# Kernel optimization log

Measured on AMD Instinct MI355X. Metric: run time of the kernel, lower is better.

Reference implementation:

```python
import math
import jax, jax.numpy as jnp
import numpy as np

B, S, D, H = 4, 1024, 1024, 16
DK = D // H
NEG = jnp.float32(-1e32)
EPS = 1e-5


def setup_inputs() -> dict:
    key = jax.random.key(0)
    ks = jax.random.split(key, 10)
    s = 1.0 / math.sqrt(D)
    return {
        "query": jax.random.normal(ks[0], (B, S, D), jnp.float32),
        "key": jax.random.normal(ks[1], (B, S, D), jnp.float32),
        "values": jax.random.normal(ks[2], (B, S, D), jnp.float32),
        "lens": jax.random.randint(ks[3], (B,), 0, S).astype(jnp.int32),
        "state_weight": jax.random.normal(ks[4], (1, H, S, S), jnp.float32),
        # params (kq_same=True -> k shares q_linear weights)
        "Wq": jax.random.normal(ks[5], (D, D), jnp.float32) * s,
        "bq": jnp.zeros((D,), jnp.float32),
        "Wv": jax.random.normal(ks[6], (D, D), jnp.float32) * s,
        "bv": jnp.zeros((D,), jnp.float32),
        "Wo": jax.random.normal(ks[7], (D, D), jnp.float32) * s,
        "bo": jnp.zeros((D,), jnp.float32),
        "gamma": jnp.ones((D,), jnp.float32),
        "beta": jnp.zeros((D,), jnp.float32),
    }


def reference(query, key, values, lens, state_weight, Wq, bq, Wv, bv, Wo, bo, gamma, beta):
    # eval-mode forward of DTransformerLayer (peek_cur=False -> strictly causal)
    b, s, d = query.shape
    mask = jnp.tril(jnp.ones((s, s), bool), -1)[None, None]  # [1,1,S,S]

    q = (query @ Wq + bq).reshape(b, s, H, DK).transpose(0, 2, 1, 3)   # bhsd
    k = (key @ Wq + bq).reshape(b, s, H, DK).transpose(0, 2, 1, 3)     # shared weights (kq_same)
    v = (values @ Wv + bv).reshape(b, s, H, DK).transpose(0, 2, 1, 3)

    scores = jnp.einsum('bhqd,bhkd->bhqk', q, k) / math.sqrt(DK)
    scores = jnp.where(mask, scores, NEG)
    scores = jnp.where(mask, scores + state_weight, NEG)
    attn = jax.nn.softmax(scores, axis=-1)
    attn = jnp.where(mask, attn, 0.0)  # fully-masked rows (row 0) -> zeros, matching torch

    ctx = jnp.einsum('bhqk,bhkd->bhqd', attn, v).transpose(0, 2, 1, 3).reshape(b, s, d)
    out = ctx @ Wo + bo

    x = query + out  # dropout is identity in eval
    mu = jnp.mean(x, axis=-1, keepdims=True)
    var = jnp.mean(jnp.square(x - mu), axis=-1, keepdims=True)
    return (x - mu) * jax.lax.rsqrt(var + EPS) * gamma + beta
```

## Files before the change

### kernel.cpp

```cpp
#include <hip/hip_runtime.h>

#define B_ 4
#define S_ 1024
#define D_ 1024
#define H_ 16
#define DK_ 64

typedef __attribute__((ext_vector_type(8))) short short8;
typedef __attribute__((ext_vector_type(4))) float f32x4;
typedef __attribute__((ext_vector_type(16))) float f32x16;

#define CBASE_PACK 0x100C090604020100ULL

static __device__ __forceinline__ unsigned bf16rne(float x) {
    unsigned b = __float_as_uint(x);
    return (b + 0x7FFFu + ((b >> 16) & 1u)) >> 16;
}

__global__ __launch_bounds__(256) void transpose_cvt3(
    const float* __restrict__ W0, const float* __restrict__ W1,
    const float* __restrict__ W2, ushort* __restrict__ T0,
    ushort* __restrict__ T1, ushort* __restrict__ T2)
{
    __shared__ float ts[32][33];
    const float* W = (blockIdx.z == 0) ? W0 : (blockIdx.z == 1) ? W1 : W2;
    ushort*     Wt = (blockIdx.z == 0) ? T0 : (blockIdx.z == 1) ? T1 : T2;
    const int t  = threadIdx.x;
    const int k0 = blockIdx.y * 32, n0 = blockIdx.x * 32;
    const int r  = t >> 3, c4 = (t & 7) * 4;
    const float4 v = *reinterpret_cast<const float4*>(&W[(size_t)(k0 + r) * 1024 + n0 + c4]);
    ts[r][c4] = v.x; ts[r][c4 + 1] = v.y; ts[r][c4 + 2] = v.z; ts[r][c4 + 3] = v.w;
    __syncthreads();
    ushort4 o;
    o.x = (ushort)bf16rne(ts[c4    ][r]);
    o.y = (ushort)bf16rne(ts[c4 + 1][r]);
    o.z = (ushort)bf16rne(ts[c4 + 2][r]);
    o.w = (ushort)bf16rne(ts[c4 + 3][r]);
    *reinterpret_cast<ushort4*>(&Wt[(size_t)(n0 + r) * 1024 + k0 + c4]) = o;
}

template<int MODE>
__global__ __launch_bounds__(256) void gemm_f32a(
    const float* __restrict__ Xf0, const float* __restrict__ Xf1,
    const ushort* __restrict__ Wt, const float* __restrict__ bias,
    void* __restrict__ out0, void* __restrict__ out1)
{
    __shared__ ushort As[2][64 * 64];
    __shared__ ushort Bs[2][128 * 64];

    const int t    = threadIdx.x;
    const int lane = t & 63;
    const int w    = t >> 6;

    const int cpx     = gridDim.x >> 3;
    const int logical = (blockIdx.x & 7) * cpx + (blockIdx.x >> 3);
    const int bm = logical >> 3;
    const int bn = logical & 7;

    const int srow   = lane >> 3;
    const int schunk = (lane & 7) ^ srow;

    const float* Xf = (MODE == 1 && bm >= 64) ? Xf1 : Xf0;
    const int rbase = (bm * 64) & 4095;
    const float* ap[2];
#pragma unroll
    for (int j = 0; j < 2; ++j)
        ap[j] = Xf + (size_t)(rbase + (j * 4 + w) * 8 + srow) * 1024 + schunk * 8;

    const ushort* bg[4];
#pragma unroll
    for (int j = 0; j < 4; ++j)
        bg[j] = Wt + (size_t)(bn * 128 + (j * 4 + w) * 8 + srow) * 1024 + schunk * 8;

    float4 aRx0, aRy0, aRx1, aRy1;

#define A_ISSUE(k0)                                                              \
    do {                                                                         \
        aRx0 = *reinterpret_cast<const float4*>(ap[0] + (k0));                   \
        aRy0 = *reinterpret_cast<const float4*>(ap[0] + (k0) + 4);               \
        aRx1 = *reinterpret_cast<const float4*>(ap[1] + (k0));                   \
        aRy1 = *reinterpret_cast<const float4*>(ap[1] + (k0) + 4);               \
    } while (0)

#define B_STAGE(buf, k0)                                                         \
    do {                                                                         \
        _Pragma("unroll")                                                        \
        for (int j = 0; j < 4; ++j)                                              \
            __builtin_amdgcn_global_load_lds(                                    \
                (__attribute__((address_space(1))) const void*)(bg[j] + (k0)),   \
                (__attribute__((address_space(3))) void*)&Bs[buf][(j * 4 + w) * 512], \
                16, 0, 0);                                                       \
    } while (0)

#define A_WRITE(buf)                                                             \
    do {                                                                         \
        union { unsigned u[4]; int4 v; } p0, p1;                                 \
        asm("v_cvt_pk_bf16_f32 %0, %1, %2" : "=v"(p0.u[0]) : "v"(aRx0.x), "v"(aRx0.y)); \
        asm("v_cvt_pk_bf16_f32 %0, %1, %2" : "=v"(p0.u[1]) : "v"(aRx0.z), "v"(aRx0.w)); \
        asm("v_cvt_pk_bf16_f32 %0, %1, %2" : "=v"(p0.u[2]) : "v"(aRy0.x), "v"(aRy0.y)); \
        asm("v_cvt_pk_bf16_f32 %0, %1, %2" : "=v"(p0.u[3]) : "v"(aRy0.z), "v"(aRy0.w)); \
        asm("v_cvt_pk_bf16_f32 %0, %1, %2" : "=v"(p1.u[0]) : "v"(aRx1.x), "v"(aRx1.y)); \
        asm("v_cvt_pk_bf16_f32 %0, %1, %2" : "=v"(p1.u[1]) : "v"(aRx1.z), "v"(aRx1.w)); \
        asm("v_cvt_pk_bf16_f32 %0, %1, %2" : "=v"(p1.u[2]) : "v"(aRy1.x), "v"(aRy1.y)); \
        asm("v_cvt_pk_bf16_f32 %0, %1, %2" : "=v"(p1.u[3]) : "v"(aRy1.z), "v"(aRy1.w)); \
        *reinterpret_cast<int4*>(&As[buf][((0 * 4 + w) * 64 + lane) * 8]) = p0.v; \
        *reinterpret_cast<int4*>(&As[buf][((1 * 4 + w) * 64 + lane) * 8]) = p1.v; \
    } while (0)

    const int fr = lane & 15;
    const int fk = lane >> 4;
    const int wm = w >> 1, wn = w & 1;

    f32x4 acc[2][4];
#pragma unroll
    for (int m = 0; m < 2; ++m)
#pragma unroll
        for (int n = 0; n < 4; ++n) acc[m][n] = (f32x4){0.f, 0.f, 0.f, 0.f};

    A_ISSUE(0);
    B_STAGE(0, 0);
    asm volatile("s_waitcnt vmcnt(4)" ::: "memory");
    A_WRITE(0);
    asm volatile("s_waitcnt lgkmcnt(0)" ::: "memory");

#pragma unroll 1
    for (int kt = 0; kt < 16; ++kt) {
        const int cur = kt & 1;
        if (kt + 1 < 16) {
            A_ISSUE((kt + 1) * 64);
            B_STAGE(cur ^ 1, (kt + 1) * 64);
            asm volatile("s_waitcnt vmcnt(8)" ::: "memory");
        } else {
            asm volatile("s_waitcnt vmcnt(0)" ::: "memory");
        }
        __builtin_amdgcn_s_barrier();
        __builtin_amdgcn_sched_barrier(0);
#pragma unroll
        for (int ks = 0; ks < 2; ++ks) {
            short8 af[2], bf[4];
#pragma unroll
            for (int m = 0; m < 2; ++m) {
                const int row = wm * 32 + m * 16 + fr;
                af[m] = *reinterpret_cast<const short8*>(
                    &As[cur][row * 64 + (((ks * 4 + fk) ^ (row & 7)) * 8)]);
            }
#pragma unroll
            for (int n = 0; n < 4; ++n) {
                const int row = wn * 64 + n * 16 + fr;
                bf[n] = *reinterpret_cast<const short8*>(
                    &Bs[cur][row * 64 + (((ks * 4 + fk) ^ (row & 7)) * 8)]);
            }
            __builtin_amdgcn_s_setprio(1);
#pragma unroll
            for (int m = 0; m < 2; ++m)
#pragma unroll
                for (int n = 0; n < 4; ++n)
                    acc[m][n] = __builtin_amdgcn_mfma_f32_16x16x32_bf16(
                        af[m], bf[n], acc[m][n], 0, 0, 0);
            __builtin_amdgcn_s_setprio(0);
        }
        if (kt + 1 < 16) {
            asm volatile("s_waitcnt vmcnt(4)" ::: "memory");
            A_WRITE(cur ^ 1);
            asm volatile("s_waitcnt lgkmcnt(0)" ::: "memory");
        }
        __builtin_amdgcn_sched_barrier(0);
        __builtin_amdgcn_s_barrier();
        __builtin_amdgcn_sched_barrier(0);
    }
#undef A_ISSUE
#undef B_STAGE
#undef A_WRITE

#pragma unroll
    for (int m = 0; m < 2; ++m) {
        const int row0 = bm * 64 + wm * 32 + m * 16 + fk * 4;
#pragma unroll
        for (int n = 0; n < 4; ++n) {
            const int col = bn * 128 + wn * 64 + n * 16 + fr;
            const float bc = bias[col];
            if (MODE == 1) {
                ushort* o = (row0 < 4096) ? (ushort*)out0 : (ushort*)out1;
                const float qs = (row0 < 4096) ? 0.125f : 1.0f;
                const int r0 = row0 & 4095;
                const int b_ = r0 >> 10, s0 = r0 & 1023;
                const int h  = col >> 6,  dk = col & 63;
#pragma unroll
                for (int j = 0; j < 4; ++j)
                    o[(((size_t)b_ * H_ + h) * S_ + s0 + j) * DK_ + dk] =
                        (ushort)bf16rne((acc[m][n][j] + bc) * qs);
            } else {
                ushort* o = (ushort*)out0;
                const int b_ = row0 >> 10, s0 = row0 & 1023;
                const int h  = col >> 6,   dk = col & 63;
                ushort4 pk;
                pk.x = (ushort)bf16rne(acc[m][n][0] + bc);
                pk.y = (ushort)bf16rne(acc[m][n][1] + bc);
                pk.z = (ushort)bf16rne(acc[m][n][2] + bc);
                pk.w = (ushort)bf16rne(acc[m][n][3] + bc);
                *reinterpret_cast<ushort4*>(
                    &o[(((size_t)b_ * H_ + h) * DK_ + dk) * S_ + s0]) = pk;
            }
        }
    }
}

__global__ __launch_bounds__(256) void gemm_bf16a(
    const ushort* __restrict__ X, const ushort* __restrict__ Wt,
    const float* __restrict__ bias, const float* __restrict__ resid,
    float* __restrict__ out)
{
    __shared__ ushort As[2][64 * 64];
    __shared__ ushort Bs[2][128 * 64];

    const int t    = threadIdx.x;
    const int lane = t & 63;
    const int w    = t >> 6;

    const int cpx     = gridDim.x >> 3;
    const int logical = (blockIdx.x & 7) * cpx + (blockIdx.x >> 3);
    const int bm = logical >> 3;
    const int bn = logical & 7;

    const int srow   = lane >> 3;
    const int schunk = (lane & 7) ^ srow;
    const ushort* ag[2];
    const ushort* bg[4];
#pragma unroll
    for (int j = 0; j < 2; ++j)
        ag[j] = X  + (size_t)(bm * 64 + (j * 4 + w) * 8 + srow) * 1024 + schunk * 8;
#pragma unroll
    for (int j = 0; j < 4; ++j)
        bg[j] = Wt + (size_t)(bn * 128 + (j * 4 + w) * 8 + srow) * 1024 + schunk * 8;

#define STAGE(buf, k0)                                                           \
    do {                                                                         \
        _Pragma("unroll")                                                        \
        for (int j = 0; j < 2; ++j)                                              \
            __builtin_amdgcn_global_load_lds(                                    \
                (__attribute__((address_space(1))) const void*)(ag[j] + (k0)),   \
                (__attribute__((address_space(3))) void*)&As[buf][(j * 4 + w) * 512], \
                16, 0, 0);                                                       \
        _Pragma("unroll")                                                        \
        for (int j = 0; j < 4; ++j)                                              \
            __builtin_amdgcn_global_load_lds(                                    \
                (__attribute__((address_space(1))) const void*)(bg[j] + (k0)),   \
                (__attribute__((address_space(3))) void*)&Bs[buf][(j * 4 + w) * 512], \
                16, 0, 0);                                                       \
    } while (0)

    const int fr = lane & 15;
    const int fk = lane >> 4;
    const int wm = w >> 1, wn = w & 1;

    f32x4 acc[2][4];
#pragma unroll
    for (int m = 0; m < 2; ++m)
#pragma unroll
        for (int n = 0; n < 4; ++n) acc[m][n] = (f32x4){0.f, 0.f, 0.f, 0.f};

    STAGE(0, 0);
#pragma unroll 1
    for (int kt = 0; kt < 16; ++kt) {
        const int cur = kt & 1;
        if (kt + 1 < 16) {
            STAGE(cur ^ 1, (kt + 1) * 64);
            asm volatile("s_waitcnt vmcnt(6)" ::: "memory");
        } else {
            asm volatile("s_waitcnt vmcnt(0)" ::: "memory");
        }
        __builtin_amdgcn_s_barrier();
        __builtin_amdgcn_sched_barrier(0);
#pragma unroll
        for (int ks = 0; ks < 2; ++ks) {
            short8 af[2], bf[4];
#pragma unroll
            for (int m = 0; m < 2; ++m) {
                const int row = wm * 32 + m * 16 + fr;
                af[m] = *reinterpret_cast<const short8*>(
                    &As[cur][row * 64 + (((ks * 4 + fk) ^ (row & 7)) * 8)]);
            }
#pragma unroll
            for (int n = 0; n < 4; ++n) {
                const int row = wn * 64 + n * 16 + fr;
                bf[n] = *reinterpret_cast<const short8*>(
                    &Bs[cur][row * 64 + (((ks * 4 + fk) ^ (row & 7)) * 8)]);
            }
            __builtin_amdgcn_s_setprio(1);
#pragma unroll
            for (int m = 0; m < 2; ++m)
#pragma unroll
                for (int n = 0; n < 4; ++n)
                    acc[m][n] = __builtin_amdgcn_mfma_f32_16x16x32_bf16(
                        af[m], bf[n], acc[m][n], 0, 0, 0);
            __builtin_amdgcn_s_setprio(0);
        }
        __builtin_amdgcn_sched_barrier(0);
        __builtin_amdgcn_s_barrier();
        __builtin_amdgcn_sched_barrier(0);
    }
#undef STAGE

#pragma unroll
    for (int m = 0; m < 2; ++m) {
        const int row0 = bm * 64 + wm * 32 + m * 16 + fk * 4;
#pragma unroll
        for (int n = 0; n < 4; ++n) {
            const int col = bn * 128 + wn * 64 + n * 16 + fr;
            const float bc = bias[col];
#pragma unroll
            for (int j = 0; j < 4; ++j) {
                const int row = row0 + j;
                out[(size_t)row * 1024 + col] =
                    acc[m][n][j] + bc + resid[(size_t)row * 1024 + col];
            }
        }
    }
}

__global__ __launch_bounds__(256) void attn_mfma(
    const ushort* __restrict__ Qh, const ushort* __restrict__ Kh,
    const ushort* __restrict__ Vt, const float* __restrict__ SW,
    ushort* __restrict__ ctxP, float2* __restrict__ ml)
{
    __shared__ ushort Ks[2][4096];
    __shared__ ushort Vs[2][4096];

    const int t    = threadIdx.x;
    const int lane = t & 63;
    const int w    = t >> 6;
    const int lg = (blockIdx.x & 7) * 160 + (blockIdx.x >> 3);
    const int b  = lg & 3;
    const int hc = lg >> 2;
    const int h  = hc / 20;
    const int ci = hc % 20;
    const int bh = b * 16 + h;
    int qb = 0;
#pragma unroll
    for (int q = 1; q < 8; ++q)
        if ((int)((CBASE_PACK >> (q * 8)) & 0xff) <= ci) qb = q;
    const int lc = ci - (int)((CBASE_PACK >> (qb * 8)) & 0xff);
    const int t0 = lc * 4;
    const int nt = min(4, 2 * qb + 2 - t0);

    const int ql = lane & 31;
    const int hi = lane >> 5;
    const int qrow = qb * 128 + ql * 4 + w;

    const ushort* Kg  = Kh + (size_t)bh * S_ * DK_;
    const ushort* Vg  = Vt + (size_t)bh * DK_ * S_;
    const float*  swp = SW + ((size_t)h * S_ + qrow) * S_;

    const ushort* kgp[2];
    const ushort* vgp[2];
#pragma unroll
    for (int j = 0; j < 2; ++j) {
        const int bb = w * 2 + j;
        const int g = bb >> 2, c = bb & 3;
        kgp[j] = Kg + (size_t)(g * 32 + ql) * DK_ + c * 16 + hi * 8;
        vgp[j] = Vg + (size_t)(g * 32 + ql) * S_  + c * 16 + hi * 8;
    }

#define ASTAGE(buf, k0)                                                          \
    do {                                                                         \
        _Pragma("unroll")                                                        \
        for (int j = 0; j < 2; ++j) {                                            \
            const int bb = w * 2 + j;                                            \
            __builtin_amdgcn_global_load_lds(                                    \
                (__attribute__((address_space(1))) const void*)(kgp[j] + (size_t)(k0) * DK_), \
                (__attribute__((address_space(3))) void*)&Ks[buf][bb * 512],     \
                16, 0, 0);                                                       \
            __builtin_amdgcn_global_load_lds(                                    \
                (__attribute__((address_space(1))) const void*)(vgp[j] + (k0)),  \
                (__attribute__((address_space(3))) void*)&Vs[buf][bb * 512],     \
                16, 0, 0);                                                       \
        }                                                                        \
    } while (0)

    short8 qf[4];
    {
        const ushort* Qg = Qh + ((size_t)bh * S_ + qrow) * DK_;
#pragma unroll
        for (int c = 0; c < 4; ++c) {
            union { int4 i; short8 s; } u;
            u.i = *reinterpret_cast<const int4*>(&Qg[c * 16 + hi * 8]);
            qf[c] = u.s;
        }
    }

    f32x16 accA, accB;
#pragma unroll
    for (int r = 0; r < 16; ++r) { accA[r] = 0.f; accB[r] = 0.f; }
    float mrow = -1e30f, lrow = 0.f;

    ASTAGE(0, t0 * 64);

#pragma unroll 1
    for (int kt = 0; kt < nt; ++kt) {
        const int cur = kt & 1;
        const int k0  = (t0 + kt) * 64;
        if (kt + 1 < nt) {
            ASTAGE(cur ^ 1, (t0 + kt + 1) * 64);
            asm volatile("s_waitcnt vmcnt(4)" ::: "memory");
        } else {
            asm volatile("s_waitcnt vmcnt(0)" ::: "memory");
        }
        __builtin_amdgcn_s_barrier();
        __builtin_amdgcn_sched_barrier(0);

        float swv[2][16];
#pragma unroll
        for (int g = 0; g < 2; ++g)
#pragma unroll
            for (int j = 0; j < 4; ++j) {
                const float4 v = *reinterpret_cast<const float4*>(
                    &swp[k0 + g * 32 + hi * 4 + j * 8]);
                swv[g][j * 4 + 0] = v.x; swv[g][j * 4 + 1] = v.y;
                swv[g][j * 4 + 2] = v.z; swv[g][j * 4 + 3] = v.w;
            }

        f32x16 sc[2];
        __builtin_amdgcn_s_setprio(1);
#pragma unroll
        for (int g = 0; g < 2; ++g) {
#pragma unroll
            for (int r = 0; r < 16; ++r) sc[g][r] = 0.f;
#pragma unroll
            for (int c = 0; c < 4; ++c) {
                const short8 kf = *reinterpret_cast<const short8*>(
                    &Ks[cur][((g * 4 + c) * 64 + lane) * 8]);
                sc[g] = __builtin_amdgcn_mfma_f32_32x32x16_bf16(kf, qf[c], sc[g], 0, 0, 0);
            }
        }
        __builtin_amdgcn_s_setprio(0);

        float pr[2][16];
        float tmax = -1e30f;
        if (t0 + kt >= 2 * qb) {
#pragma unroll
            for (int g = 0; g < 2; ++g)
#pragma unroll
                for (int r = 0; r < 16; ++r) {
                    const int key = k0 + g * 32 + (r & 3) + ((r >> 2) << 3) + (hi << 2);
                    const float s = (key < qrow) ? sc[g][r] + swv[g][r] : -1e30f;
                    pr[g][r] = s;
                    tmax = fmaxf(tmax, s);
                }
        } else {
#pragma unroll
            for (int g = 0; g < 2; ++g)
#pragma unroll
                for (int r = 0; r < 16; ++r) {
                    const float s = sc[g][r] + swv[g][r];
                    pr[g][r] = s;
                    tmax = fmaxf(tmax, s);
                }
        }
        tmax = fmaxf(tmax, __shfl_xor(tmax, 32, 64));
        const float mnew = fmaxf(mrow, tmax);
        const float corr = __expf(mrow - mnew);
        float psum = 0.f;
#pragma unroll
        for (int g = 0; g < 2; ++g)
#pragma unroll
            for (int r = 0; r < 16; ++r) {
                const float e = (pr[g][r] > -1e29f) ? __expf(pr[g][r] - mnew) : 0.f;
                pr[g][r] = e;
                psum += e;
            }
        psum += __shfl_xor(psum, 32, 64);
        lrow = lrow * corr + psum;
        mrow = mnew;
#pragma unroll
        for (int r = 0; r < 16; ++r) { accA[r] *= corr; accB[r] *= corr; }

        short8 paf[4];
#pragma unroll
        for (int g = 0; g < 2; ++g) {
            unsigned pk[8];
#pragma unroll
            for (int j = 0; j < 8; ++j) {
                unsigned r_;
                asm("v_cvt_pk_bf16_f32 %0, %1, %2"
                    : "=v"(r_) : "v"(pr[g][2 * j]), "v"(pr[g][2 * j + 1]));
                pk[j] = r_;
            }
            unsigned x0 = (unsigned)__shfl_xor((int)pk[0], 32, 64);
            unsigned x1 = (unsigned)__shfl_xor((int)pk[1], 32, 64);
            unsigned x2 = (unsigned)__shfl_xor((int)pk[2], 32, 64);
            unsigned x3 = (unsigned)__shfl_xor((int)pk[3], 32, 64);
            unsigned x4 = (unsigned)__shfl_xor((int)pk[4], 32, 64);
            unsigned x5 = (unsigned)__shfl_xor((int)pk[5], 32, 64);
            unsigned x6 = (unsigned)__shfl_xor((int)pk[6], 32, 64);
            unsigned x7 = (unsigned)__shfl_xor((int)pk[7], 32, 64);
            union { unsigned u[4]; short8 s; } a0, a1;
            a0.u[0] = hi ? x2 : pk[0];
            a0.u[1] = hi ? x3 : pk[1];
            a0.u[2] = hi ? pk[2] : x0;
            a0.u[3] = hi ? pk[3] : x1;
            a1.u[0] = hi ? x6 : pk[4];
            a1.u[1] = hi ? x7 : pk[5];
            a1.u[2] = hi ? pk[6] : x4;
            a1.u[3] = hi ? pk[7] : x5;
            paf[g * 2 + 0] = a0.s;
            paf[g * 2 + 1] = a1.s;
        }

        __builtin_amdgcn_s_setprio(1);
#pragma unroll
        for (int cc = 0; cc < 4; ++cc) {
            const short8 va = *reinterpret_cast<const short8*>(
                &Vs[cur][((0 * 4 + cc) * 64 + lane) * 8]);
            const short8 vb = *reinterpret_cast<const short8*>(
                &Vs[cur][((1 * 4 + cc) * 64 + lane) * 8]);
            accA = __builtin_amdgcn_mfma_f32_32x32x16_bf16(va, paf[cc], accA, 0, 0, 0);
            accB = __builtin_amdgcn_mfma_f32_32x32x16_bf16(vb, paf[cc], accB, 0, 0, 0);
        }
        __builtin_amdgcn_s_setprio(0);

        __builtin_amdgcn_sched_barrier(0);
        __builtin_amdgcn_s_barrier();
        __builtin_amdgcn_sched_barrier(0);
    }
#undef ASTAGE

    const float inv = (lrow > 0.f) ? 1.f / lrow : 0.f;
    ushort* crow_ = ctxP + ((size_t)(bh * 20 + ci) * 128 + (ql * 4 + w)) * 64;
#pragma unroll
    for (int g = 0; g < 4; ++g) {
        ushort4 oA, oB;
        oA.x = (ushort)bf16rne(accA[4 * g + 0] * inv);
        oA.y = (ushort)bf16rne(accA[4 * g + 1] * inv);
        oA.z = (ushort)bf16rne(accA[4 * g + 2] * inv);
        oA.w = (ushort)bf16rne(accA[4 * g + 3] * inv);
        oB.x = (ushort)bf16rne(accB[4 * g + 0] * inv);
        oB.y = (ushort)bf16rne(accB[4 * g + 1] * inv);
        oB.z = (ushort)bf16rne(accB[4 * g + 2] * inv);
        oB.w = (ushort)bf16rne(accB[4 * g + 3] * inv);
        *reinterpret_cast<ushort4*>(&crow_[g * 8 + hi * 4])      = oA;
        *reinterpret_cast<ushort4*>(&crow_[g * 8 + hi * 4 + 32]) = oB;
    }
    if (hi == 0) {
        float2 v; v.x = mrow; v.y = lrow;
        ml[(size_t)(bh * 20 + ci) * 128 + ql * 4 + w] = v;
    }
}

__global__ __launch_bounds__(256) void attn_merge(
    const ushort* __restrict__ ctxP, const float2* __restrict__ ml,
    ushort* __restrict__ ctx)
{
    const size_t idx = ((size_t)blockIdx.x * 256 + threadIdx.x) * 8;
    const int col = (int)(idx & 1023);
    const int row = (int)(idx >> 10);
    const int b = row >> 10, s = row & 1023;
    const int h = col >> 6, dk0 = col & 63;
    const int bh = b * 16 + h;
    const int qb = s >> 7, rl = s & 127;
    const int nch = (qb + 2) >> 1;
    const int cb  = (int)((CBASE_PACK >> (qb * 8)) & 0xff);

    float mm[4], ll[4];
    float m = -1e30f;
#pragma unroll
    for (int c = 0; c < 4; ++c)
        if (c < nch) {
            const float2 v = ml[(size_t)(bh * 20 + cb + c) * 128 + rl];
            mm[c] = v.x; ll[c] = v.y;
            m = fmaxf(m, v.x);
        }
    float wc[4], wsum = 0.f;
#pragma unroll
    for (int c = 0; c < 4; ++c)
        if (c < nch) { wc[c] = ll[c] * __expf(mm[c] - m); wsum += wc[c]; }
    const float inv = (wsum > 0.f) ? 1.f / wsum : 0.f;

    float o[8] = {0.f, 0.f, 0.f, 0.f, 0.f, 0.f, 0.f, 0.f};
#pragma unroll
    for (int c = 0; c < 4; ++c)
        if (c < nch) {
            union { int4 v; ushort u[8]; } p;
            p.v = *reinterpret_cast<const int4*>(
                &ctxP[((size_t)(bh * 20 + cb + c) * 128 + rl) * 64 + dk0]);
            const float wgt = wc[c] * inv;
#pragma unroll
            for (int i = 0; i < 8; ++i)
                o[i] += wgt * __uint_as_float((unsigned)p.u[i] << 16);
        }
    union { int4 v; ushort u[8]; } r;
#pragma unroll
    for (int i = 0; i < 8; ++i) r.u[i] = (ushort)bf16rne(o[i]);
    *reinterpret_cast<int4*>(ctx + idx) = r.v;
}

__global__ __launch_bounds__(256) void layernorm_k(
    const float* __restrict__ x, const float* __restrict__ gamma,
    const float* __restrict__ beta, float* __restrict__ out)
{
    const int row = blockIdx.x;
    const int t   = threadIdx.x;
    const float4 v = *reinterpret_cast<const float4*>(&x[(size_t)row * D_ + (t << 2)]);
    float sum = v.x + v.y + v.z + v.w;
    float sq  = v.x * v.x + v.y * v.y + v.z * v.z + v.w * v.w;
#pragma unroll
    for (int w = 1; w < 64; w <<= 1) {
        sum += __shfl_xor(sum, w, 64);
        sq  += __shfl_xor(sq,  w, 64);
    }
    __shared__ float red[8];
    const int wid = t >> 6;
    if ((t & 63) == 0) { red[wid] = sum; red[wid + 4] = sq; }
    __syncthreads();
    sum = red[0] + red[1] + red[2] + red[3];
    sq  = red[4] + red[5] + red[6] + red[7];
    const float mu  = sum * (1.f / 1024.f);
    const float var = sq * (1.f / 1024.f) - mu * mu;
    const float rs  = rsqrtf(var + 1e-5f);
    const float4 gm = *reinterpret_cast<const float4*>(&gamma[t << 2]);
    const float4 bt = *reinterpret_cast<const float4*>(&beta[t << 2]);
    float4 o;
    o.x = (v.x - mu) * rs * gm.x + bt.x;
    o.y = (v.y - mu) * rs * gm.y + bt.y;
    o.z = (v.z - mu) * rs * gm.z + bt.z;
    o.w = (v.w - mu) * rs * gm.w + bt.w;
    *reinterpret_cast<float4*>(&out[(size_t)row * D_ + (t << 2)]) = o;
}

extern "C" void kernel_launch(void* const* d_in, const int* in_sizes, int n_in,
                              void* d_out, int out_size, void* d_ws, size_t ws_size,
                              hipStream_t stream)
{
    const float* query  = (const float*)d_in[0];
    const float* key    = (const float*)d_in[1];
    const float* values = (const float*)d_in[2];
    const float* SW     = (const float*)d_in[4];
    const float* Wq     = (const float*)d_in[5];
    const float* bq     = (const float*)d_in[6];
    const float* Wv     = (const float*)d_in[7];
    const float* bv     = (const float*)d_in[8];
    const float* Wo     = (const float*)d_in[9];
    const float* bo     = (const float*)d_in[10];
    const float* gamma  = (const float*)d_in[11];
    const float* beta   = (const float*)d_in[12];

    char* ws = (char*)d_ws;
    const size_t MB = 1024 * 1024;
    ushort* Qh   = (ushort*)(ws);
    ushort* Kh   = (ushort*)(ws +  8 * MB);
    ushort* Vt   = (ushort*)(ws + 16 * MB);
    ushort* Wqt  = (ushort*)(ws + 24 * MB);
    ushort* Wvt  = (ushort*)(ws + 26 * MB);
    ushort* Wot  = (ushort*)(ws + 28 * MB);
    ushort* ctxP = (ushort*)(ws + 30 * MB);
    float2* ml   = (float2*)(ws + 52 * MB);
    ushort* ctxm = Qh;
    float*  xbf  = (float*)(ws + 8 * MB);

    const dim3 blk(256);

    transpose_cvt3<<<dim3(32, 32, 3), blk, 0, stream>>>(Wq, Wv, Wo, Wqt, Wvt, Wot);

    gemm_f32a<1><<<dim3(1024), blk, 0, stream>>>(query, key, Wqt, bq, Qh, Kh);
    gemm_f32a<2><<<dim3(512),  blk, 0, stream>>>(values, nullptr, Wvt, bv, Vt, nullptr);

    attn_mfma<<<dim3(1280), blk, 0, stream>>>(Qh, Kh, Vt, SW, ctxP, ml);
    attn_merge<<<dim3(2048), blk, 0, stream>>>(ctxP, ml, ctxm);

    gemm_bf16a<<<dim3(512), blk, 0, stream>>>(ctxm, Wot, bo, query, xbf);

    layernorm_k<<<dim3(4096), blk, 0, stream>>>(xbf, gamma, beta, (float*)d_out);
}
```

Before: 145.0 us.

## Fuse Q/K/V projections into one launch and rebalance causal attention chunking

The separate Q/K and V projection GEMM launches become a single kernel of 1536 blocks that picks its input, weight, bias and output layout from the block's row index. This removes one launch and lets the V tiles fill the machine alongside Q/K. The attention split-K decomposition changes from 20 chunks per head to 16, using packed lookup tables for query block, start tile and tile count. This reduces the block count and merge work and is meant to balance causal work per block better. The risk lies in the per-chunk tile counts and in the merge tables having to match the new partition exactly.

After: 127.7 us. 11.9% less time.

```diff
diff --git a/kernel.cpp b/kernel.cpp
--- a/kernel.cpp
+++ b/kernel.cpp
@@ -10,7 +10,11 @@
 typedef __attribute__((ext_vector_type(4))) float f32x4;
 typedef __attribute__((ext_vector_type(16))) float f32x16;
 
-#define CBASE_PACK 0x100C090604020100ULL
+#define QBPACK 0x7777666554433210ULL
+#define T0PACK 0xC840A50605040000ULL
+#define NTPACK 0x4444455665544642ULL
+#define CBPACK  0x0C09070503020100ULL
+#define NCHPACK 0x43222111U
 
 static __device__ __forceinline__ unsigned bf16rne(float x) {
     unsigned b = __float_as_uint(x);
@@ -39,11 +43,12 @@
     *reinterpret_cast<ushort4*>(&Wt[(size_t)(n0 + r) * 1024 + k0 + c4]) = o;
 }
 
-template<int MODE>
-__global__ __launch_bounds__(256) void gemm_f32a(
-    const float* __restrict__ Xf0, const float* __restrict__ Xf1,
-    const ushort* __restrict__ Wt, const float* __restrict__ bias,
-    void* __restrict__ out0, void* __restrict__ out1)
+__global__ __launch_bounds__(256) void gemm_qkv(
+    const float* __restrict__ q, const float* __restrict__ k,
+    const float* __restrict__ v, const ushort* __restrict__ Wqt,
+    const ushort* __restrict__ Wvt, const float* __restrict__ bq,
+    const float* __restrict__ bv, ushort* __restrict__ Qh,
+    ushort* __restrict__ Kh, ushort* __restrict__ Vt)
 {
     __shared__ ushort As[2][64 * 64];
     __shared__ ushort Bs[2][128 * 64];
@@ -57,11 +62,14 @@
     const int bm = logical >> 3;
     const int bn = logical & 7;
 
+    const int mode = bm >> 6;
+    const float* Xf = (mode == 0) ? q : (mode == 1) ? k : v;
+    const ushort* Wt = (mode == 2) ? Wvt : Wqt;
+    const float* bias = (mode == 2) ? bv : bq;
+    const int rbase = (bm & 63) * 64;
+
     const int srow   = lane >> 3;
     const int schunk = (lane & 7) ^ srow;
-
-    const float* Xf = (MODE == 1 && bm >= 64) ? Xf1 : Xf0;
-    const int rbase = (bm * 64) & 4095;
     const float* ap[2];
 #pragma unroll
     for (int j = 0; j < 2; ++j)
@@ -174,32 +182,31 @@
 
 #pragma unroll
     for (int m = 0; m < 2; ++m) {
-        const int row0 = bm * 64 + wm * 32 + m * 16 + fk * 4;
+        const int row0 = rbase + wm * 32 + m * 16 + fk * 4;
 #pragma unroll
         for (int n = 0; n < 4; ++n) {
             const int col = bn * 128 + wn * 64 + n * 16 + fr;
             const float bc = bias[col];
-            if (MODE == 1) {
-                ushort* o = (row0 < 4096) ? (ushort*)out0 : (ushort*)out1;
-                const float qs = (row0 < 4096) ? 0.125f : 1.0f;
-                const int r0 = row0 & 4095;
-                const int b_ = r0 >> 10, s0 = r0 & 1023;
-                const int h  = col >> 6,  dk = col & 63;
+            const int b_ = row0 >> 10, s0 = row0 & 1023;
+            const int h  = col >> 6,   dk = col & 63;
+            if (mode == 0) {
 #pragma unroll
                 for (int j = 0; j < 4; ++j)
-                    o[(((size_t)b_ * H_ + h) * S_ + s0 + j) * DK_ + dk] =
-                        (ushort)bf16rne((acc[m][n][j] + bc) * qs);
+                    Qh[(((size_t)b_ * H_ + h) * S_ + s0 + j) * DK_ + dk] =
+                        (ushort)bf16rne((acc[m][n][j] + bc) * 0.125f);
+            } else if (mode == 1) {
+#pragma unroll
+                for (int j = 0; j < 4; ++j)
+                    Kh[(((size_t)b_ * H_ + h) * S_ + s0 + j) * DK_ + dk] =
+                        (ushort)bf16rne(acc[m][n][j] + bc);
             } else {
-                ushort* o = (ushort*)out0;
-                const int b_ = row0 >> 10, s0 = row0 & 1023;
-                const int h  = col >> 6,   dk = col & 63;
                 ushort4 pk;
                 pk.x = (ushort)bf16rne(acc[m][n][0] + bc);
                 pk.y = (ushort)bf16rne(acc[m][n][1] + bc);
                 pk.z = (ushort)bf16rne(acc[m][n][2] + bc);
                 pk.w = (ushort)bf16rne(acc[m][n][3] + bc);
                 *reinterpret_cast<ushort4*>(
-                    &o[(((size_t)b_ * H_ + h) * DK_ + dk) * S_ + s0]) = pk;
+                    &Vt[(((size_t)b_ * H_ + h) * DK_ + dk) * S_ + s0]) = pk;
             }
         }
     }
@@ -329,19 +336,15 @@
     const int t    = threadIdx.x;
     const int lane = t & 63;
     const int w    = t >> 6;
-    const int lg = (blockIdx.x & 7) * 160 + (blockIdx.x >> 3);
+    const int lg = (blockIdx.x & 7) * 128 + (blockIdx.x >> 3);
     const int b  = lg & 3;
     const int hc = lg >> 2;
-    const int h  = hc / 20;
-    const int ci = hc % 20;
+    const int h  = hc >> 4;
+    const int ci = hc & 15;
     const int bh = b * 16 + h;
-    int qb = 0;
-#pragma unroll
-    for (int q = 1; q < 8; ++q)
-        if ((int)((CBASE_PACK >> (q * 8)) & 0xff) <= ci) qb = q;
-    const int lc = ci - (int)((CBASE_PACK >> (qb * 8)) & 0xff);
-    const int t0 = lc * 4;
-    const int nt = min(4, 2 * qb + 2 - t0);
+    const int qb = (int)((QBPACK >> (ci * 4)) & 15);
+    const int t0 = (int)((T0PACK >> (ci * 4)) & 15);
+    const int nt = (int)((NTPACK >> (ci * 4)) & 15);
 
     const int ql = lane & 31;
     const int hi = lane >> 5;
@@ -525,7 +528,7 @@
 #undef ASTAGE
 
     const float inv = (lrow > 0.f) ? 1.f / lrow : 0.f;
-    ushort* crow_ = ctxP + ((size_t)(bh * 20 + ci) * 128 + (ql * 4 + w)) * 64;
+    ushort* crow_ = ctxP + ((size_t)(bh * 16 + ci) * 128 + (ql * 4 + w)) * 64;
 #pragma unroll
     for (int g = 0; g < 4; ++g) {
         ushort4 oA, oB;
@@ -542,7 +545,7 @@
     }
     if (hi == 0) {
         float2 v; v.x = mrow; v.y = lrow;
-        ml[(size_t)(bh * 20 + ci) * 128 + ql * 4 + w] = v;
+        ml[(size_t)(bh * 16 + ci) * 128 + ql * 4 + w] = v;
     }
 }
 
@@ -557,15 +560,15 @@
     const int h = col >> 6, dk0 = col & 63;
     const int bh = b * 16 + h;
     const int qb = s >> 7, rl = s & 127;
-    const int nch = (qb + 2) >> 1;
-    const int cb  = (int)((CBASE_PACK >> (qb * 8)) & 0xff);
+    const int nch = (int)((NCHPACK >> (qb * 4)) & 15);
+    const int cb  = (int)((CBPACK >> (qb * 8)) & 255);
 
     float mm[4], ll[4];
     float m = -1e30f;
 #pragma unroll
     for (int c = 0; c < 4; ++c)
         if (c < nch) {
-            const float2 v = ml[(size_t)(bh * 20 + cb + c) * 128 + rl];
+            const float2 v = ml[(size_t)(bh * 16 + cb + c) * 128 + rl];
             mm[c] = v.x; ll[c] = v.y;
             m = fmaxf(m, v.x);
         }
@@ -581,7 +584,7 @@
         if (c < nch) {
             union { int4 v; ushort u[8]; } p;
             p.v = *reinterpret_cast<const int4*>(
-                &ctxP[((size_t)(bh * 20 + cb + c) * 128 + rl) * 64 + dk0]);
+                &ctxP[((size_t)(bh * 16 + cb + c) * 128 + rl) * 64 + dk0]);
             const float wgt = wc[c] * inv;
 #pragma unroll
             for (int i = 0; i < 8; ++i)
@@ -652,7 +655,7 @@
     ushort* Wvt  = (ushort*)(ws + 26 * MB);
     ushort* Wot  = (ushort*)(ws + 28 * MB);
     ushort* ctxP = (ushort*)(ws + 30 * MB);
-    float2* ml   = (float2*)(ws + 52 * MB);
+    float2* ml   = (float2*)(ws + 46 * MB);
     ushort* ctxm = Qh;
     float*  xbf  = (float*)(ws + 8 * MB);
 
@@ -660,10 +663,10 @@
 
     transpose_cvt3<<<dim3(32, 32, 3), blk, 0, stream>>>(Wq, Wv, Wo, Wqt, Wvt, Wot);
 
-    gemm_f32a<1><<<dim3(1024), blk, 0, stream>>>(query, key, Wqt, bq, Qh, Kh);
-    gemm_f32a<2><<<dim3(512),  blk, 0, stream>>>(values, nullptr, Wvt, bv, Vt, nullptr);
-
-    attn_mfma<<<dim3(1280), blk, 0, stream>>>(Qh, Kh, Vt, SW, ctxP, ml);
+    gemm_qkv<<<dim3(1536), blk, 0, stream>>>(query, key, values, Wqt, Wvt,
+                                             bq, bv, Qh, Kh, Vt);
+
+    attn_mfma<<<dim3(1024), blk, 0, stream>>>(Qh, Kh, Vt, SW, ctxP, ml);
     attn_merge<<<dim3(2048), blk, 0, stream>>>(ctxP, ml, ctxm);
 
     gemm_bf16a<<<dim3(512), blk, 0, stream>>>(ctxm, Wot, bo, query, xbf);
```
